# Performance work log

Hardware: AMD Instinct MI355X
Metric: run time of the kernel (lower is better)

## Reference

```python
import jax, jax.numpy as jnp
import numpy as np

D_MODEL = 1024
NHEAD = 16
HEAD_DIM = D_MODEL // NHEAD
WINDOW = 64


def setup_inputs() -> dict:
    key = jax.random.key(0)
    ks = jax.random.split(key, 5)
    B, S = 1, 4096
    x = jax.random.normal(ks[0], (B, S, D_MODEL), dtype=jnp.float32)
    scale = 0.02
    Wq = jax.random.normal(ks[1], (D_MODEL, D_MODEL), dtype=jnp.float32) * scale
    Wk = jax.random.normal(ks[2], (D_MODEL, D_MODEL), dtype=jnp.float32) * scale
    Wv = jax.random.normal(ks[3], (D_MODEL, D_MODEL), dtype=jnp.float32) * scale
    Wo = jax.random.normal(ks[4], (D_MODEL, D_MODEL), dtype=jnp.float32) * scale
    return {"x": x, "Wq": Wq, "Wk": Wk, "Wv": Wv, "Wo": Wo}


def reference(x, Wq, Wk, Wv, Wo):
    B, S, D = x.shape
    H, hd, W = NHEAD, HEAD_DIM, WINDOW
    # projections (torch Linear: y = x @ W.T)
    q = (x @ Wq.T).reshape(B, S, H, hd).transpose(0, 2, 1, 3)  # [B,H,S,hd]
    k = (x @ Wk.T).reshape(B, S, H, hd).transpose(0, 2, 1, 3)
    v = (x @ Wv.T).reshape(B, S, H, hd).transpose(0, 2, 1, 3)
    # sliding window indices: each query attends to [i-W+1, i]
    qpos = jnp.arange(S)
    offsets = jnp.arange(-W + 1, 1)
    key_idx = qpos[:, None] + offsets[None, :]          # [S,W]
    valid = (key_idx >= 0) & (key_idx < S)
    key_idx = jnp.clip(key_idx, 0, S - 1)
    # gather windows: [B,H,S,W,hd]
    kw = jnp.take(k, key_idx, axis=2)
    vw = jnp.take(v, key_idx, axis=2)
    scores = jnp.einsum('bhsd,bhswd->bhsw', q, kw) / (hd ** 0.5)
    scores = jnp.where(valid[None, None, :, :], scores, -jnp.inf)
    attn = jax.nn.softmax(scores, axis=-1)
    out = jnp.einsum('bhsw,bhswd->bhsd', attn, vw)      # [B,H,S,hd]
    out = out.transpose(0, 2, 1, 3).reshape(B, S, D)
    return out @ Wo.T
```

## Files before the change

kernel.cpp:

```cpp
#include <hip/hip_runtime.h>
#include <cstdint>

typedef unsigned short u16;
using bf16x8 = __attribute__((ext_vector_type(8))) short;
using u16x8  = __attribute__((ext_vector_type(8))) unsigned short;
using f32x4  = __attribute__((ext_vector_type(4))) float;

#define DM 1024

__device__ __forceinline__ u16 f2b(float f) {
    union { float f; unsigned u; } v; v.f = f;
    unsigned r = v.u + 0x7FFFu + ((v.u >> 16) & 1u);
    return (u16)(r >> 16);
}
__device__ __forceinline__ float b2f(u16 b) {
    union { unsigned u; float f; } v; v.u = ((unsigned)b) << 16;
    return v.f;
}

#define GLL(gp, lp) __builtin_amdgcn_global_load_lds( \
    (const __attribute__((address_space(1))) void*)(uintptr_t)(gp), \
    (__attribute__((address_space(3))) void*)(unsigned)(uintptr_t)(lp), 16, 0, 0)

#define BAR()    __builtin_amdgcn_s_barrier()
#define WAITV3() asm volatile("s_waitcnt vmcnt(3)" ::: "memory")
#define WAITV0() asm volatile("s_waitcnt vmcnt(0)" ::: "memory")

__global__ __launch_bounds__(256) void cvt_all(const float* __restrict__ x,
                                               const float* __restrict__ Wq,
                                               const float* __restrict__ Wk,
                                               const float* __restrict__ Wv,
                                               const float* __restrict__ Wo,
                                               u16* __restrict__ xb,
                                               u16* __restrict__ wqkv,
                                               u16* __restrict__ wob) {
    size_t v = ((size_t)blockIdx.x * 256 + threadIdx.x) << 3;
    const float* src; u16* dst; size_t off;
    if (v < (size_t)4194304) { src = x; dst = xb; off = v; }
    else {
        size_t w = v - 4194304; int s = (int)(w >> 20); off = w & 1048575;
        src = (s == 0) ? Wq : (s == 1) ? Wk : (s == 2) ? Wv : Wo;
        dst = (s < 3) ? (wqkv + ((size_t)s << 20)) : wob;
    }
    const f32x4* p = (const f32x4*)(src + off);
    f32x4 a = p[0], b = p[1];
    u16x8 o;
    o[0] = f2b(a[0]); o[1] = f2b(a[1]); o[2] = f2b(a[2]); o[3] = f2b(a[3]);
    o[4] = f2b(b[0]); o[5] = f2b(b[1]); o[6] = f2b(b[2]); o[7] = f2b(b[3]);
    *(u16x8*)(dst + off) = o;
}

#define MROW3(af_, bf_, d) \
    acc[d][0] = __builtin_amdgcn_mfma_f32_16x16x32_bf16(af_, bf_[0], acc[d][0], 0, 0, 0); \
    acc[d][1] = __builtin_amdgcn_mfma_f32_16x16x32_bf16(af_, bf_[1], acc[d][1], 0, 0, 0); \
    acc[d][2] = __builtin_amdgcn_mfma_f32_16x16x32_bf16(af_, bf_[2], acc[d][2], 0, 0, 0);

#define MFMA12(af_, bf_, ib) do { \
    __builtin_amdgcn_s_setprio(1); \
    MROW3(af_[0], bf_, (ib) + 0) \
    MROW3(af_[1], bf_, (ib) + 1) \
    MROW3(af_[2], bf_, (ib) + 2) \
    MROW3(af_[3], bf_, (ib) + 3) \
    __builtin_amdgcn_s_setprio(0); } while (0)

__global__ __launch_bounds__(512, 2) void gemm_qkv8(const u16* __restrict__ A,
                                                    const u16* __restrict__ B,
                                                    u16* __restrict__ QKV) {
    __shared__ __align__(16) u16 As[2 * 16384];
    __shared__ __align__(16) u16 Bs[2 * 12288];
    const int tid  = threadIdx.x;
    const int lane = tid & 63;
    const int wid  = tid >> 6;
    const int wr   = wid >> 2;
    const int wc   = wid & 3;
    const int fr   = lane & 15;
    const int fg   = lane >> 4;

    const int hw   = blockIdx.y * 16 + blockIdx.x;
    const int lg   = (hw & 7) * 32 + (hw >> 3);
    const int brow = (lg >> 4) << 8;
    const int bcol = (lg & 15) * 192;

    const int srow = tid >> 3;
    const int scol = ((tid & 7) ^ (srow & 7)) << 3;
    const u16* Ag = A + (size_t)(brow + srow) * 1024 + scol;
    const u16* Bg = B + (size_t)(bcol + srow) * 1024 + scol;

#define STG_A(buf, kt, c) GLL(Ag + (size_t)(c) * 65536 + (kt) * 64, \
                              (char*)As + (buf) * 32768 + (c) * 8192 + (wid << 10))
#define STG_B(buf, kt, c) GLL(Bg + (size_t)(c) * 65536 + (kt) * 64, \
                              (char*)Bs + (buf) * 24576 + (c) * 8192 + (wid << 10))

    const int swz  = (fr & 7) << 3;
    const int col0 = (fg << 3) ^ swz;
    const int col1 = (32 + (fg << 3)) ^ swz;
    const int aro  = ((wr << 7) + fr) << 6;
    const int bro  = ((wc * 48) + fr) << 6;

#define LDA4(dst, bufo, ih, cl) do { \
    const u16* p_ = As + (bufo) + aro + ((ih) << 12) + (cl); \
    dst[0] = *(const bf16x8*)(p_); \
    dst[1] = *(const bf16x8*)(p_ + 1024); \
    dst[2] = *(const bf16x8*)(p_ + 2048); \
    dst[3] = *(const bf16x8*)(p_ + 3072); } while (0)

#define LDB3(dst, bufo, cl) do { \
    const u16* p_ = Bs + (bufo) + bro + (cl); \
    dst[0] = *(const bf16x8*)(p_); \
    dst[1] = *(const bf16x8*)(p_ + 1024); \
    dst[2] = *(const bf16x8*)(p_ + 2048); } while (0)

    f32x4 acc[8][3];
    const f32x4 z = {0.f, 0.f, 0.f, 0.f};
    #pragma unroll
    for (int i = 0; i < 8; ++i)
        #pragma unroll
        for (int j = 0; j < 3; ++j) acc[i][j] = z;

    bf16x8 af0[4], af1[4], bf0[3], bf1[3];

    STG_B(0, 0, 0); STG_B(0, 0, 1); STG_B(0, 0, 2);
    STG_A(0, 0, 0); STG_A(0, 0, 1); STG_A(0, 0, 2); STG_A(0, 0, 3);
    STG_B(1, 1, 0); STG_B(1, 1, 1); STG_B(1, 1, 2);
    WAITV3();
    BAR();

    #pragma unroll 1
    for (int t = 0; t < 7; ++t) {
        const int k1 = 2 * t + 1, k2 = 2 * t + 2, k3 = 2 * t + 3;
        LDA4(af0, 0, 0, col0); LDB3(bf0, 0, col0);
        STG_A(1, k1, 0); STG_A(1, k1, 1);
        BAR(); MFMA12(af0, bf0, 0); BAR();
        LDA4(af1, 0, 0, col1); LDB3(bf1, 0, col1);
        STG_A(1, k1, 2); STG_A(1, k1, 3);
        BAR(); MFMA12(af1, bf1, 0); BAR();
        LDA4(af0, 0, 1, col0);
        STG_B(0, k2, 0); STG_B(0, k2, 1);
        BAR(); MFMA12(af0, bf0, 4); BAR();
        LDA4(af1, 0, 1, col1);
        STG_B(0, k2, 2);
        BAR(); MFMA12(af1, bf1, 4); WAITV3(); BAR();
        LDA4(af0, 16384, 0, col0); LDB3(bf0, 12288, col0);
        STG_A(0, k2, 0); STG_A(0, k2, 1);
        BAR(); MFMA12(af0, bf0, 0); BAR();
        LDA4(af1, 16384, 0, col1); LDB3(bf1, 12288, col1);
        STG_A(0, k2, 2); STG_A(0, k2, 3);
        BAR(); MFMA12(af1, bf1, 0); BAR();
        LDA4(af0, 16384, 1, col0);
        STG_B(1, k3, 0); STG_B(1, k3, 1);
        BAR(); MFMA12(af0, bf0, 4); BAR();
        LDA4(af1, 16384, 1, col1);
        STG_B(1, k3, 2);
        BAR(); MFMA12(af1, bf1, 4); WAITV3(); BAR();
    }
    LDA4(af0, 0, 0, col0); LDB3(bf0, 0, col0);
    STG_A(1, 15, 0); STG_A(1, 15, 1);
    BAR(); MFMA12(af0, bf0, 0); BAR();
    LDA4(af1, 0, 0, col1); LDB3(bf1, 0, col1);
    STG_A(1, 15, 2); STG_A(1, 15, 3);
    BAR(); MFMA12(af1, bf1, 0); BAR();
    LDA4(af0, 0, 1, col0);
    BAR(); MFMA12(af0, bf0, 4); BAR();
    LDA4(af1, 0, 1, col1);
    BAR(); MFMA12(af1, bf1, 4); WAITV0(); BAR();
    LDA4(af0, 16384, 0, col0); LDB3(bf0, 12288, col0);
    BAR(); MFMA12(af0, bf0, 0); BAR();
    LDA4(af1, 16384, 0, col1); LDB3(bf1, 12288, col1);
    BAR(); MFMA12(af1, bf1, 0); BAR();
    LDA4(af0, 16384, 1, col0);
    BAR(); MFMA12(af0, bf0, 4); BAR();
    LDA4(af1, 16384, 1, col1);
    BAR(); MFMA12(af1, bf1, 4);

    const int ocol0 = bcol + wc * 48;
    const int orow0 = brow + (wr << 7);
    #pragma unroll
    for (int i = 0; i < 8; ++i)
        #pragma unroll
        for (int j = 0; j < 3; ++j)
            #pragma unroll
            for (int r = 0; r < 4; ++r) {
                const int row = orow0 + i * 16 + fg * 4 + r;
                const int col = ocol0 + j * 16 + fr;
                QKV[(size_t)row * 3072 + col] = f2b(acc[i][j][r]);
            }
#undef STG_A
#undef STG_B
#undef LDA4
#undef LDB3
}

__device__ __forceinline__ void gemm_core_1024(const u16* __restrict__ A,
                                               const u16* __restrict__ B,
                                               int brow, int bcol,
                                               u16* Asb, u16* Bsb,
                                               f32x4 acc[4][4]) {
    const int tid  = threadIdx.x;
    const int lane = tid & 63;
    const int wid  = tid >> 6;
    const int wrow = (wid >> 1) << 6;
    const int wcol = (wid & 1) << 6;
    const int fr   = lane & 15;
    const int fk   = (lane >> 4) << 3;

    const size_t aBase = (size_t)(brow + (tid >> 2)) * 1024 + ((tid & 3) << 3);
    const size_t bBase = (size_t)(bcol + (tid >> 2)) * 1024 + ((tid & 3) << 3);
    const int wOff = wid << 10;

    const f32x4 z = {0.f, 0.f, 0.f, 0.f};
    #pragma unroll
    for (int i = 0; i < 4; ++i)
        #pragma unroll
        for (int j = 0; j < 4; ++j) acc[i][j] = z;

#define STAGE(bufi, kt) do { \
        const u16* ga_ = A + aBase + ((size_t)(kt) << 5); \
        const u16* gb_ = B + bBase + ((size_t)(kt) << 5); \
        char* la_ = (char*)(Asb + ((bufi) << 12)) + wOff; \
        char* lb_ = (char*)(Bsb + ((bufi) << 12)) + wOff; \
        GLL(ga_, la_); GLL(ga_ + (size_t)64 * 1024, la_ + 4096); \
        GLL(gb_, lb_); GLL(gb_ + (size_t)64 * 1024, lb_ + 4096); \
    } while (0)

    STAGE(0, 0);
    #pragma unroll 2
    for (int kt = 0; kt < 32; ++kt) {
        const int buf = kt & 1;
        __syncthreads();
        if (kt + 1 < 32) STAGE(buf ^ 1, kt + 1);
        const u16* As = Asb + (buf << 12);
        const u16* Bs = Bsb + (buf << 12);
        bf16x8 af[4], bfr[4];
        #pragma unroll
        for (int i = 0; i < 4; ++i)
            af[i] = *(const bf16x8*)(As + ((wrow + (i << 4) + fr) << 5) + fk);
        #pragma unroll
        for (int j = 0; j < 4; ++j)
            bfr[j] = *(const bf16x8*)(Bs + ((wcol + (j << 4) + fr) << 5) + fk);
        #pragma unroll
        for (int i = 0; i < 4; ++i)
            #pragma unroll
            for (int j = 0; j < 4; ++j)
                acc[i][j] = __builtin_amdgcn_mfma_f32_16x16x32_bf16(af[i], bfr[j], acc[i][j], 0, 0, 0);
    }
#undef STAGE
}

__global__ __launch_bounds__(256) void gemm_out(const u16* __restrict__ A,
                                                const u16* __restrict__ B,
                                                float* __restrict__ C) {
    __shared__ __align__(16) u16 As[2 * 128 * 32];
    __shared__ __align__(16) u16 Bs[2 * 128 * 32];
    const int brow = blockIdx.y << 7;
    const int bcol = blockIdx.x << 7;
    f32x4 acc[4][4];
    gemm_core_1024(A, B, brow, bcol, As, Bs, acc);

    const int lane = threadIdx.x & 63;
    const int wid  = threadIdx.x >> 6;
    const int wrow = (wid >> 1) << 6;
    const int wcol = (wid & 1) << 6;
    const int g = lane >> 4, c = lane & 15;
    #pragma unroll
    for (int i = 0; i < 4; ++i)
        #pragma unroll
        for (int j = 0; j < 4; ++j)
            #pragma unroll
            for (int r = 0; r < 4; ++r) {
                const int row = brow + wrow + i * 16 + g * 4 + r;
                const int col = bcol + wcol + j * 16 + c;
                C[(size_t)row * 1024 + col] = acc[i][j][r];
            }
}

__global__ __launch_bounds__(256) void attn_kernel(const u16* __restrict__ QKV,
                                                   u16* __restrict__ Og) {
    const int qb  = blockIdx.x;
    const int h   = blockIdx.y;
    const int tid = threadIdx.x;
    const int lane = tid & 63;
    const int w  = tid >> 6;
    const int fr = lane & 15;
    const int fg = lane >> 4;

    __shared__ __align__(16) u16 QK[64 * 72 + 128 * 72];
    __shared__ __align__(16) u16 Vt[64 * 138];
    __shared__ float Mrow[64][4];
    __shared__ float Lrow[64][4];

    u16* Qs = QK;
    u16* Ks = QK + 64 * 72;
    u16* Ps = QK;

    const u16* Qg = QKV;
    const u16* Kg = QKV + 1024;
    const u16* Vg = QKV + 2048;

    const int hoff  = h * 64;
    const int qrow0 = qb * 64;
    const int krow0 = qrow0 - 64;

    {
        const int r  = tid >> 3;
        const int c0 = (tid & 7) * 8;
        #pragma unroll
        for (int it = 0; it < 2; ++it) {
            const int row = r + it * 32;
            u16x8 val = *(const u16x8*)(Qg + (size_t)(qrow0 + row) * 3072 + hoff + c0);
            u16x8 o;
            #pragma unroll
            for (int e = 0; e < 8; ++e) o[e] = f2b(b2f(val[e]) * 0.125f);
            *(u16x8*)(Qs + row * 72 + c0) = o;
        }
        #pragma unroll
        for (int it = 0; it < 4; ++it) {
            const int row  = r + it * 32;
            const int grow = krow0 + row;
            u16x8 val = {0, 0, 0, 0, 0, 0, 0, 0};
            if (grow >= 0) val = *(const u16x8*)(Kg + (size_t)grow * 3072 + hoff + c0);
            *(u16x8*)(Ks + row * 72 + c0) = val;
        }
        #pragma unroll
        for (int it = 0; it < 4; ++it) {
            const int j    = r + it * 32;
            const int grow = krow0 + j;
            u16x8 val = {0, 0, 0, 0, 0, 0, 0, 0};
            if (grow >= 0) val = *(const u16x8*)(Vg + (size_t)grow * 3072 + hoff + c0);
            #pragma unroll
            for (int e = 0; e < 8; ++e) Vt[(c0 + e) * 138 + j] = val[e];
        }
    }
    __syncthreads();

    const f32x4 z = {0.f, 0.f, 0.f, 0.f};
    f32x4 s[4][2];
    #pragma unroll
    for (int i = 0; i < 4; ++i) { s[i][0] = z; s[i][1] = z; }
    #pragma unroll
    for (int kk = 0; kk < 2; ++kk) {
        const int k0 = kk * 32 + fg * 8;
        bf16x8 aq[4];
        #pragma unroll
        for (int i = 0; i < 4; ++i)
            aq[i] = *(const bf16x8*)(Qs + (i * 16 + fr) * 72 + k0);
        #pragma unroll
        for (int n = 0; n < 2; ++n) {
            const bf16x8 bk = *(const bf16x8*)(Ks + (w * 32 + n * 16 + fr) * 72 + k0);
            #pragma unroll
            for (int i = 0; i < 4; ++i)
                s[i][n] = __builtin_amdgcn_mfma_f32_16x16x32_bf16(aq[i], bk, s[i][n], 0, 0, 0);
        }
    }

    #pragma unroll
    for (int i = 0; i < 4; ++i) {
        #pragma unroll
        for (int r = 0; r < 4; ++r) {
            const int irow = i * 16 + fg * 4 + r;
            float mx = -3.0e38f;
            #pragma unroll
            for (int n = 0; n < 2; ++n) {
                const int jcol = w * 32 + n * 16 + fr;
                const bool valid = (jcol >= irow + 1) && (jcol <= irow + 64) && (krow0 + jcol >= 0);
                const float v = valid ? s[i][n][r] : -3.0e38f;
                s[i][n][r] = v;
                mx = fmaxf(mx, v);
            }
            #pragma unroll
            for (int d = 1; d < 16; d <<= 1) mx = fmaxf(mx, __shfl_xor(mx, d));
            if (fr == 0) Mrow[irow][w] = mx;
        }
    }
    __syncthreads();

    #pragma unroll
    for (int i = 0; i < 4; ++i) {
        #pragma unroll
        for (int r = 0; r < 4; ++r) {
            const int irow = i * 16 + fg * 4 + r;
            const float M = fmaxf(fmaxf(Mrow[irow][0], Mrow[irow][1]),
                                  fmaxf(Mrow[irow][2], Mrow[irow][3]));
            float sum = 0.f;
            #pragma unroll
            for (int n = 0; n < 2; ++n) {
                const float v = s[i][n][r];
                const float p = (v > -1.0e38f) ? __expf(v - M) : 0.f;
                sum += p;
                Ps[irow * 136 + (w * 32 + n * 16 + fr)] = f2b(p);
            }
            #pragma unroll
            for (int d = 1; d < 16; d <<= 1) sum += __shfl_xor(sum, d);
            if (fr == 0) Lrow[irow][w] = sum;
        }
    }
    __syncthreads();

    f32x4 o[4] = {z, z, z, z};
    #pragma unroll
    for (int ks = 0; ks < 4; ++ks) {
        const int k0 = ks * 32 + fg * 8;
        const bf16x8 ap = *(const bf16x8*)(Ps + (w * 16 + fr) * 136 + k0);
        #pragma unroll
        for (int n = 0; n < 4; ++n) {
            const bf16x8 bv = *(const bf16x8*)(Vt + (n * 16 + fr) * 138 + k0);
            o[n] = __builtin_amdgcn_mfma_f32_16x16x32_bf16(ap, bv, o[n], 0, 0, 0);
        }
    }

    #pragma unroll
    for (int r = 0; r < 4; ++r) {
        const int irow = w * 16 + fg * 4 + r;
        const float L = Lrow[irow][0] + Lrow[irow][1] + Lrow[irow][2] + Lrow[irow][3];
        const float rl = 1.0f / L;
        #pragma unroll
        for (int n = 0; n < 4; ++n)
            Og[(size_t)(qrow0 + irow) * DM + hoff + n * 16 + fr] = f2b(o[n][r] * rl);
    }
}

extern "C" void kernel_launch(void* const* d_in, const int* in_sizes, int n_in,
                              void* d_out, int out_size, void* d_ws, size_t ws_size,
                              hipStream_t stream) {
    (void)in_sizes; (void)n_in; (void)out_size; (void)ws_size;
    const float* x  = (const float*)d_in[0];
    const float* Wq = (const float*)d_in[1];
    const float* Wk = (const float*)d_in[2];
    const float* Wv = (const float*)d_in[3];
    const float* Wo = (const float*)d_in[4];
    float* out = (float*)d_out;

    char* ws = (char*)d_ws;
    u16* xb   = (u16*)(ws);
    u16* Wqkv = (u16*)(ws + ((size_t)8  << 20));
    u16* Wob  = (u16*)(ws + ((size_t)14 << 20));
    u16* qkvb = (u16*)(ws + ((size_t)16 << 20));
    u16* ab   = (u16*)(ws + ((size_t)40 << 20));

    cvt_all<<<4096, 256, 0, stream>>>(x, Wq, Wk, Wv, Wo, xb, Wqkv, Wob);
    gemm_qkv8<<<dim3(16, 16), 512, 0, stream>>>(xb, Wqkv, qkvb);
    attn_kernel<<<dim3(64, 16), 256, 0, stream>>>(qkvb, ab);
    gemm_out<<<dim3(8, 32), 256, 0, stream>>>(ab, Wob, out);
}
```

Measured before the change: 85.67 us.

## Retile output projection GEMM to 128x64 tiles with BK=64 and swizzled LDS

```diff
diff --git a/kernel.cpp b/kernel.cpp
--- a/kernel.cpp
+++ b/kernel.cpp
@@ -190,85 +190,87 @@
 #undef LDB3
 }
 
-__device__ __forceinline__ void gemm_core_1024(const u16* __restrict__ A,
-                                               const u16* __restrict__ B,
-                                               int brow, int bcol,
-                                               u16* Asb, u16* Bsb,
-                                               f32x4 acc[4][4]) {
+__global__ __launch_bounds__(256) void gemm_out(const u16* __restrict__ A,
+                                                const u16* __restrict__ B,
+                                                float* __restrict__ C) {
+    __shared__ __align__(16) u16 As[2 * 8192];
+    __shared__ __align__(16) u16 Bs[2 * 4096];
     const int tid  = threadIdx.x;
     const int lane = tid & 63;
     const int wid  = tid >> 6;
-    const int wrow = (wid >> 1) << 6;
-    const int wcol = (wid & 1) << 6;
+    const int wr   = wid >> 1;
+    const int wc   = wid & 1;
     const int fr   = lane & 15;
-    const int fk   = (lane >> 4) << 3;
-
-    const size_t aBase = (size_t)(brow + (tid >> 2)) * 1024 + ((tid & 3) << 3);
-    const size_t bBase = (size_t)(bcol + (tid >> 2)) * 1024 + ((tid & 3) << 3);
-    const int wOff = wid << 10;
-
+    const int fg   = lane >> 4;
+
+    const int hw   = blockIdx.y * 16 + blockIdx.x;
+    const int lg   = (hw & 7) * 64 + (hw >> 3);
+    const int brow = (lg >> 4) << 7;
+    const int bcol = (lg & 15) << 6;
+
+    const int srow = tid >> 3;
+    const int scol = ((tid & 7) ^ (srow & 7)) << 3;
+    const u16* Ag = A + (size_t)(brow + srow) * 1024 + scol;
+    const u16* Bg = B + (size_t)(bcol + srow) * 1024 + scol;
+
+#define OSTG_A(buf, kt, c) GLL(Ag + (size_t)(c) * 32768 + (kt) * 64, \
+                               (char*)As + (buf) * 16384 + (c) * 4096 + (tid << 4))
+#define OSTG_B(buf, kt, c) GLL(Bg + (size_t)(c) * 32768 + (kt) * 64, \
+                               (char*)Bs + (buf) * 8192 + (c) * 4096 + (tid << 4))
+#define OSTG(buf, kt) do { \
+        OSTG_A(buf, kt, 0); OSTG_A(buf, kt, 1); OSTG_A(buf, kt, 2); OSTG_A(buf, kt, 3); \
+        OSTG_B(buf, kt, 0); OSTG_B(buf, kt, 1); } while (0)
+
+    const int swz  = (fr & 7) << 3;
+    const int col0 = (fg << 3) ^ swz;
+    const int col1 = (32 + (fg << 3)) ^ swz;
+    const int aro  = ((wr << 6) + fr) << 6;
+    const int bro  = ((wc << 5) + fr) << 6;
+
+    f32x4 acc[4][2];
     const f32x4 z = {0.f, 0.f, 0.f, 0.f};
     #pragma unroll
-    for (int i = 0; i < 4; ++i)
-        #pragma unroll
-        for (int j = 0; j < 4; ++j) acc[i][j] = z;
-
-#define STAGE(bufi, kt) do { \
-        const u16* ga_ = A + aBase + ((size_t)(kt) << 5); \
-        const u16* gb_ = B + bBase + ((size_t)(kt) << 5); \
-        char* la_ = (char*)(Asb + ((bufi) << 12)) + wOff; \
-        char* lb_ = (char*)(Bsb + ((bufi) << 12)) + wOff; \
-        GLL(ga_, la_); GLL(ga_ + (size_t)64 * 1024, la_ + 4096); \
-        GLL(gb_, lb_); GLL(gb_ + (size_t)64 * 1024, lb_ + 4096); \
-    } while (0)
-
-    STAGE(0, 0);
+    for (int i = 0; i < 4; ++i) { acc[i][0] = z; acc[i][1] = z; }
+
+    OSTG(0, 0);
     #pragma unroll 2
-    for (int kt = 0; kt < 32; ++kt) {
+    for (int kt = 0; kt < 16; ++kt) {
         const int buf = kt & 1;
         __syncthreads();
-        if (kt + 1 < 32) STAGE(buf ^ 1, kt + 1);
-        const u16* As = Asb + (buf << 12);
-        const u16* Bs = Bsb + (buf << 12);
-        bf16x8 af[4], bfr[4];
+        if (kt + 1 < 16) OSTG(buf ^ 1, kt + 1);
+        const u16* Ab = As + (buf << 13);
+        const u16* Bb = Bs + (buf << 12);
+        bf16x8 a0[4], a1[4], b0[2], b1[2];
+        #pragma unroll
+        for (int i = 0; i < 4; ++i) {
+            a0[i] = *(const bf16x8*)(Ab + aro + (i << 10) + col0);
+            a1[i] = *(const bf16x8*)(Ab + aro + (i << 10) + col1);
+        }
+        #pragma unroll
+        for (int j = 0; j < 2; ++j) {
+            b0[j] = *(const bf16x8*)(Bb + bro + (j << 10) + col0);
+            b1[j] = *(const bf16x8*)(Bb + bro + (j << 10) + col1);
+        }
         #pragma unroll
         for (int i = 0; i < 4; ++i)
-            af[i] = *(const bf16x8*)(As + ((wrow + (i << 4) + fr) << 5) + fk);
-        #pragma unroll
-        for (int j = 0; j < 4; ++j)
-            bfr[j] = *(const bf16x8*)(Bs + ((wcol + (j << 4) + fr) << 5) + fk);
-        #pragma unroll
-        for (int i = 0; i < 4; ++i)
-            #pragma unroll
-            for (int j = 0; j < 4; ++j)
-                acc[i][j] = __builtin_amdgcn_mfma_f32_16x16x32_bf16(af[i], bfr[j], acc[i][j], 0, 0, 0);
-    }
-#undef STAGE
-}
-
-__global__ __launch_bounds__(256) void gemm_out(const u16* __restrict__ A,
-                                                const u16* __restrict__ B,
-                                                float* __restrict__ C) {
-    __shared__ __align__(16) u16 As[2 * 128 * 32];
-    __shared__ __align__(16) u16 Bs[2 * 128 * 32];
-    const int brow = blockIdx.y << 7;
-    const int bcol = blockIdx.x << 7;
-    f32x4 acc[4][4];
-    gemm_core_1024(A, B, brow, bcol, As, Bs, acc);
-
-    const int lane = threadIdx.x & 63;
-    const int wid  = threadIdx.x >> 6;
-    const int wrow = (wid >> 1) << 6;
-    const int wcol = (wid & 1) << 6;
-    const int g = lane >> 4, c = lane & 15;
+            #pragma unroll
+            for (int j = 0; j < 2; ++j) {
+                acc[i][j] = __builtin_amdgcn_mfma_f32_16x16x32_bf16(a0[i], b0[j], acc[i][j], 0, 0, 0);
+                acc[i][j] = __builtin_amdgcn_mfma_f32_16x16x32_bf16(a1[i], b1[j], acc[i][j], 0, 0, 0);
+            }
+    }
+#undef OSTG_A
+#undef OSTG_B
+#undef OSTG
+
     #pragma unroll
     for (int i = 0; i < 4; ++i)
         #pragma unroll
-        for (int j = 0; j < 4; ++j)
+        for (int j = 0; j < 2; ++j)
             #pragma unroll
             for (int r = 0; r < 4; ++r) {
-                const int row = brow + wrow + i * 16 + g * 4 + r;
-                const int col = bcol + wcol + j * 16 + c;
+                const int row = brow + wr * 64 + i * 16 + fg * 4 + r;
+                const int col = bcol + wc * 32 + j * 16 + fr;
                 C[(size_t)row * 1024 + col] = acc[i][j][r];
             }
 }
@@ -439,5 +441,5 @@
     cvt_all<<<4096, 256, 0, stream>>>(x, Wq, Wk, Wv, Wo, xb, Wqkv, Wob);
     gemm_qkv8<<<dim3(16, 16), 512, 0, stream>>>(xb, Wqkv, qkvb);
     attn_kernel<<<dim3(64, 16), 256, 0, stream>>>(qkvb, ab);
-    gemm_out<<<dim3(8, 32), 256, 0, stream>>>(ab, Wob, out);
-}
+    gemm_out<<<dim3(16, 32), 256, 0, stream>>>(ab, Wob, out);
+}
```

Result: faster. 80.79 us (-5.7%).
